# Optimization experiments

Measured on AMD Instinct MI355X. Metric: run time of the kernel, lower is better.

Reference implementation:

```python
import jax, jax.numpy as jnp
import numpy as np
from jax import lax

# ---- Haar (db1) wavelet filters, matching create_wavelet_filter ----
_S2 = float(1.0 / np.sqrt(2.0))
_dec_lo = np.array([_S2, _S2], np.float32)    # pywt dec_lo reversed (symmetric)
_dec_hi = np.array([_S2, -_S2], np.float32)   # pywt dec_hi [-s,s] reversed
_rec_lo = np.array([_S2, _S2], np.float32)    # pywt rec_lo flipped (symmetric)
_rec_hi = np.array([-_S2, _S2], np.float32)   # pywt rec_hi [s,-s] flipped

def _outer(a, b):  # torch: a.unsqueeze(0) * b.unsqueeze(1) -> [i,j] = a[j]*b[i]
    return b[:, None] * a[None, :]

DEC = jnp.asarray(np.stack([_outer(_dec_lo, _dec_lo), _outer(_dec_lo, _dec_hi),
                            _outer(_dec_hi, _dec_lo), _outer(_dec_hi, _dec_hi)]))  # [4,2,2]
REC = jnp.asarray(np.stack([_outer(_rec_lo, _rec_lo), _outer(_rec_lo, _rec_hi),
                            _outer(_rec_hi, _rec_lo), _outer(_rec_hi, _rec_hi)]))  # [4,2,2]

BN_EPS = 1e-5

def mish(x):
    return x * jnp.tanh(jax.nn.softplus(x))

def silu(x):
    return x * jax.nn.sigmoid(x)

def bn(x, g, b):  # eval-mode BatchNorm2d with running_mean=0, running_var=1
    return x * (g / jnp.sqrt(1.0 + BN_EPS))[None, :, None, None] + b[None, :, None, None]

def dwconv(x, w, pad):  # depthwise conv, w: [C,1,k,k]
    return lax.conv_general_dilated(x, w, (1, 1), [(pad, pad), (pad, pad)],
                                    feature_group_count=x.shape[1],
                                    dimension_numbers=('NCHW', 'OIHW', 'NCHW'))

def dyn_dwconv(x, ew, gw):
    # DynamicConv2d (depthwise experts). ew: [E,C,1,k,k], gw: [E,C]
    gates = jax.nn.softmax(x.mean((2, 3)) @ gw.T, axis=-1)  # [B,E]
    k = ew.shape[-1]
    outs = jnp.stack([dwconv(x, ew[e], k // 2) for e in range(ew.shape[0])], 1)  # [B,E,C,H,W]
    return jnp.einsum('be,bechw->bchw', gates, outs)

def local_branch(x, ew, gw, bn1g, bn1b, pw, bn2g, bn2b):
    # DWConv2d_BN_ReLU: dynamic dwconv -> BN -> Mish -> depthwise 1x1 (per-channel scale) -> BN
    y = mish(bn(dyn_dwconv(x, ew, gw), bn1g, bn1b))
    y = y * pw[None, :, None, None]
    return bn(y, bn2g, bn2b)

def sel_scan(u, xw, dtw, dtb, Alog, Dp):
    # u: [B,L,D]; xw: [R+2N,D]; dtw: [D,R]; dtb: [D]; Alog: [D,N]; Dp: [D]
    R = dtw.shape[1]
    N = Alog.shape[1]
    xdbl = jnp.einsum('bld,ed->ble', u, xw)
    dt, Bm, Cm = xdbl[..., :R], xdbl[..., R:R + N], xdbl[..., R + N:]
    delta = jax.nn.softplus(jnp.einsum('blr,dr->bld', dt, dtw) + dtb)  # [B,L,D]
    A = -jnp.exp(Alog)                                                  # [D,N]
    a = jnp.exp(delta[..., None] * A)                                   # [B,L,D,N]
    b = delta[..., None] * Bm[:, :, None, :] * u[..., None]             # [B,L,D,N]
    def comb(c1, c2):
        a1, b1 = c1
        a2, b2 = c2
        return a1 * a2, a2 * b1 + b2
    _, h = lax.associative_scan(comb, (a, b), axis=1)                    # h_t = a_t h_{t-1} + b_t
    return jnp.einsum('bldn,bln->bld', h, Cm) + Dp * u

def ss2d(x, in_w, cw, cb, xpw, dtw, dtb, Alog, Dp, ow):
    # SS2D (d_state=1, k_group=2, channel_first): in_proj -> dwconv+silu -> 2-direction
    # selective scan -> gate with silu(z) -> out_proj.
    B, C, H, W = x.shape
    xz = jnp.einsum('oc,bchw->bohw', in_w, x)
    d = in_w.shape[0] // 2
    xi, z = xz[:, :d], xz[:, d:]
    xc = silu(dwconv(xi, cw, 1) + cb[None, :, None, None])
    u0 = xc.reshape(B, d, H * W).transpose(0, 2, 1)                       # row-major scan
    u1 = xc.transpose(0, 1, 3, 2).reshape(B, d, H * W).transpose(0, 2, 1)  # col-major scan
    y0 = sel_scan(u0, xpw[0], dtw[0], dtb[0], Alog[0], Dp[0])
    y1 = sel_scan(u1, xpw[1], dtw[1], dtb[1], Alog[1], Dp[1])
    y0 = y0.transpose(0, 2, 1).reshape(B, d, H, W)
    y1 = y1.transpose(0, 2, 1).reshape(B, d, W, H).transpose(0, 1, 3, 2)
    y = (y0 + y1) * silu(z)
    return jnp.einsum('oc,bchw->bohw', ow, y)

def mbwt(x, wav_w, wav_b, wav_scale, base_scale,
         ss_in_w, ss_conv_w, ss_conv_b, ss_xproj_w, ss_dt_w, ss_dt_b, ss_A_log, ss_D, ss_out_w):
    # MBWTConv2d, wt_levels=1, H/W even. Haar WT (2x2 stride 2) == block reshape + einsum.
    B, C, H, W = x.shape
    xr = x.reshape(B, C, H // 2, 2, W // 2, 2)
    wt = jnp.einsum('bchpwq,kpq->bckhw', xr, DEC)                  # [B,C,4,h,w]
    tag = wt.reshape(B, 4 * C, H // 2, W // 2)
    tag = dwconv(tag, wav_w, wav_w.shape[-1] // 2) + wav_b[None, :, None, None]
    tag = (tag * wav_scale).reshape(B, C, 4, H // 2, W // 2)
    # inverse Haar WT (conv_transpose 2x2 stride 2, groups=C)
    up = jnp.einsum('bckhw,kpq->bchpwq', tag, REC).reshape(B, C, H, W)
    g = ss2d(x, ss_in_w, ss_conv_w, ss_conv_b, ss_xproj_w, ss_dt_w, ss_dt_b, ss_A_log, ss_D, ss_out_w)
    return base_scale * g + up


def setup_inputs() -> dict:
    key = jax.random.key(0)
    ks = iter(jax.random.split(key, 64))
    B, DIM, H, W = 16, 256, 64, 64
    Cg = Cl = 64
    d = {'x': jax.random.normal(next(ks), (B, DIM, H, W), jnp.float32)}
    for j, k in enumerate((3, 5, 7)):
        p = f'l{j}_'
        d[p + 'ew'] = jax.random.normal(next(ks), (4, Cl, 1, k, k), jnp.float32) * 0.1
        d[p + 'gw'] = jax.random.normal(next(ks), (4, Cl), jnp.float32) * 0.1
        d[p + 'bn1g'] = jnp.ones((Cl,), jnp.float32)
        d[p + 'bn1b'] = jnp.zeros((Cl,), jnp.float32)
        d[p + 'pw'] = jax.random.normal(next(ks), (Cl,), jnp.float32) * 0.2
        d[p + 'bn2g'] = jnp.ones((Cl,), jnp.float32)
        d[p + 'bn2b'] = jnp.zeros((Cl,), jnp.float32)
    d['wav_w'] = jax.random.normal(next(ks), (4 * Cg, 1, 3, 3), jnp.float32) * 0.1
    d['wav_b'] = jnp.zeros((4 * Cg,), jnp.float32)
    d['wav_scale'] = jnp.full((1, 4 * Cg, 1, 1), 0.1, jnp.float32)
    d['base_scale'] = jnp.ones((1, Cg, 1, 1), jnp.float32)
    dm, R, N, K = Cg, 4, 1, 2  # d_inner, dt_rank, d_state, k_group
    d['ss_in_w'] = jax.random.normal(next(ks), (2 * dm, Cg), jnp.float32) * float(1 / np.sqrt(Cg))
    d['ss_conv_w'] = jax.random.normal(next(ks), (dm, 1, 3, 3), jnp.float32) * 0.1
    d['ss_conv_b'] = jnp.zeros((dm,), jnp.float32)
    d['ss_xproj_w'] = jax.random.normal(next(ks), (K, R + 2 * N, dm), jnp.float32) * float(1 / np.sqrt(dm))
    d['ss_dt_w'] = jax.random.normal(next(ks), (K, dm, R), jnp.float32) * float(1 / np.sqrt(R))
    d['ss_dt_b'] = jnp.full((K, dm), -2.0, jnp.float32)
    d['ss_A_log'] = jnp.zeros((K, dm, N), jnp.float32)
    d['ss_D'] = jnp.ones((K, dm), jnp.float32)
    d['ss_out_w'] = jax.random.normal(next(ks), (Cg, dm), jnp.float32) * float(1 / np.sqrt(dm))
    return d


def reference(x,
              l0_ew, l0_gw, l0_bn1g, l0_bn1b, l0_pw, l0_bn2g, l0_bn2b,
              l1_ew, l1_gw, l1_bn1g, l1_bn1b, l1_pw, l1_bn2g, l1_bn2b,
              l2_ew, l2_gw, l2_bn1g, l2_bn1b, l2_pw, l2_bn2g, l2_bn2b,
              wav_w, wav_b, wav_scale, base_scale,
              ss_in_w, ss_conv_w, ss_conv_b, ss_xproj_w, ss_dt_w, ss_dt_b, ss_A_log, ss_D, ss_out_w):
    Cg, Cl = 64, 64
    xg, xl, xi = x[:, :Cg], x[:, Cg:Cg + Cl], x[:, Cg + Cl:]
    yl = (local_branch(xl, l0_ew, l0_gw, l0_bn1g, l0_bn1b, l0_pw, l0_bn2g, l0_bn2b)
          + local_branch(xl, l1_ew, l1_gw, l1_bn1g, l1_bn1b, l1_pw, l1_bn2g, l1_bn2b)
          + local_branch(xl, l2_ew, l2_gw, l2_bn1g, l2_bn1b, l2_pw, l2_bn2g, l2_bn2b))
    yg = mbwt(xg, wav_w, wav_b, wav_scale, base_scale,
              ss_in_w, ss_conv_w, ss_conv_b, ss_xproj_w, ss_dt_w, ss_dt_b, ss_A_log, ss_D, ss_out_w)
    return jnp.concatenate([yg, yl, xi], axis=1)
```

## Files before the change

kernel.cpp:

```cpp
#include <hip/hip_runtime.h>
#include <math.h>

static constexpr int NB   = 16;
static constexpr int DIM  = 256;
static constexpr int CG   = 64;
static constexpr int HH   = 64;
static constexpr int WW   = 64;
static constexpr int HW   = HH * WW;

__device__ __forceinline__ float mish_fast(float x) {
    float t = __expf(fminf(x, 20.f));
    float p = __builtin_fmaf(t, t, t + t);
    return x * p * __builtin_amdgcn_rcpf(p + 2.f);
}
__device__ __forceinline__ float silu_f(float x) {
    return x * __builtin_amdgcn_rcpf(1.f + __expf(-x));
}
__device__ __forceinline__ float softplus_fast(float x) {
    return fmaxf(x, 0.f) + __logf(1.f + __expf(-fabsf(x)));
}

__global__ __launch_bounds__(256) void k_stage1(
    const float* __restrict__ x,
    const float* __restrict__ wav_w, const float* __restrict__ wav_b,
    const float* __restrict__ wav_scale,
    float* __restrict__ up, float* __restrict__ mean,
    const float* __restrict__ in_w,
    float* __restrict__ xi, float* __restrict__ z) {
    __shared__ float smem[8192];
    int bid = blockIdx.x;
    int tid = threadIdx.x;

    if (bid % 3 != 2) {
        int aid = (bid / 3) * 2 + (bid % 3);
        int c = aid & 63, b = aid >> 6;
        float* wtb = smem;
        float* red = smem + 4352;
        const float* xp = x + ((size_t)b * DIM + c) * HW;

        {
            const float4* lp4 = (const float4*)(x + ((size_t)b * DIM + 64 + c) * HW);
            float s = 0.f;
            for (int i = tid; i < 1024; i += 256) {
                float4 v = lp4[i];
                s += (v.x + v.y) + (v.z + v.w);
            }
#pragma unroll
            for (int off = 32; off > 0; off >>= 1) s += __shfl_xor(s, off, 64);
            if ((tid & 63) == 0) red[tid >> 6] = s;
            __syncthreads();
            if (tid == 0)
                mean[b * 64 + c] = ((red[0] + red[1]) + (red[2] + red[3])) * (1.f / HW);
        }

#pragma unroll
        for (int it = 0; it < 2; ++it) {
            int p = tid + it * 256;
            int h = p >> 4, w2 = p & 15;
            float4 top = *(const float4*)(xp + (2 * h) * 64 + 4 * w2);
            float4 bot = *(const float4*)(xp + (2 * h + 1) * 64 + 4 * w2);
            float a0 = top.x, b0 = top.y, c0q = bot.x, d0 = bot.y;
            float a1 = top.z, b1 = top.w, c1q = bot.z, d1 = bot.w;
            int base0 = h * 34 + 2 * w2;
            *(float2*)(wtb + 0 * 1088 + base0) =
                make_float2(0.5f * (a0 + b0 + c0q + d0), 0.5f * (a1 + b1 + c1q + d1));
            *(float2*)(wtb + 1 * 1088 + base0) =
                make_float2(0.5f * (a0 + b0 - c0q - d0), 0.5f * (a1 + b1 - c1q - d1));
            *(float2*)(wtb + 2 * 1088 + base0) =
                make_float2(0.5f * (a0 - b0 + c0q - d0), 0.5f * (a1 - b1 + c1q - d1));
            *(float2*)(wtb + 3 * 1088 + base0) =
                make_float2(0.5f * (a0 - b0 - c0q + d0), 0.5f * (a1 - b1 - c1q + d1));
        }
        __syncthreads();

        float wk[4][9], tb[4];
#pragma unroll
        for (int k = 0; k < 4; ++k) {
            int ch = c * 4 + k;
            float sc = wav_scale[ch];
#pragma unroll
            for (int j = 0; j < 9; ++j) wk[k][j] = wav_w[ch * 9 + j] * sc;
            tb[k] = wav_b[ch] * sc;
        }
        float* upp = up + ((size_t)b * CG + c) * HW;
        for (int i = tid; i < 1024; i += 256) {
            int h = i >> 5, w = i & 31;
            float tg[4];
#pragma unroll
            for (int k = 0; k < 4; ++k) {
                float s = tb[k];
#pragma unroll
                for (int dy = -1; dy <= 1; ++dy) {
                    int hh = h + dy;
                    if (hh < 0 || hh >= 32) continue;
#pragma unroll
                    for (int dx = -1; dx <= 1; ++dx) {
                        int wx = w + dx;
                        if (wx < 0 || wx >= 32) continue;
                        s = fmaf(wtb[k * 1088 + hh * 34 + wx], wk[k][(dy + 1) * 3 + (dx + 1)], s);
                    }
                }
                tg[k] = s;
            }
            float u00 = 0.5f * (tg[0] - tg[1] - tg[2] + tg[3]);
            float u01 = 0.5f * (tg[0] - tg[1] + tg[2] - tg[3]);
            float u10 = 0.5f * (tg[0] + tg[1] - tg[2] - tg[3]);
            float u11 = 0.5f * (tg[0] + tg[1] + tg[2] + tg[3]);
            *(float2*)(upp + (2 * h) * 64 + 2 * w)     = make_float2(u00, u01);
            *(float2*)(upp + (2 * h + 1) * 64 + 2 * w) = make_float2(u10, u11);
        }
    } else {
        int id2 = bid / 3;
        int h0 = (id2 & 31) * 2;
        int b  = id2 >> 5;
        float* xs = smem;
        float* wt = smem + 4096;

        float acc[8][8];
#pragma unroll
        for (int i = 0; i < 8; ++i)
#pragma unroll
            for (int j = 0; j < 8; ++j) acc[i][j] = 0.f;

        int o0 = (tid >> 4) * 8;
        int p0 = (tid & 15) * 8;

        for (int ko = 0; ko < 64; ko += 32) {
            if (ko) __syncthreads();
            {
                int s = tid;
#pragma unroll
                for (int it = 0; it < 4; ++it, s += 256) {
                    int c = s >> 5, p4 = (s & 31) * 4;
                    float4 v = *(const float4*)(x + ((size_t)b * DIM + ko + c) * HW + h0 * 64 + p4);
                    *(float4*)(xs + c * 128 + p4) = v;
                }
            }
            {
                int s = tid;
#pragma unroll
                for (int it = 0; it < 4; ++it, s += 256) {
                    int o = s >> 3, c0 = (s & 7) * 4;
#pragma unroll
                    for (int i = 0; i < 4; ++i) {
                        int cc = c0 + i;
                        int osw = o ^ (((cc >> 2) & 3) << 3);
                        wt[cc * 128 + osw] = ((const float*)(in_w + o * 64 + ko + c0))[i];
                    }
                }
            }
            __syncthreads();
#pragma unroll 4
            for (int c = 0; c < 32; ++c) {
                int osw = o0 ^ (((c >> 2) & 3) << 3);
                float xv[8], wv[8];
                *(float4*)(xv)     = *(const float4*)(xs + c * 128 + p0);
                *(float4*)(xv + 4) = *(const float4*)(xs + c * 128 + p0 + 4);
                *(float4*)(wv)     = *(const float4*)(wt + c * 128 + osw);
                *(float4*)(wv + 4) = *(const float4*)(wt + c * 128 + osw + 4);
#pragma unroll
                for (int i = 0; i < 8; ++i)
#pragma unroll
                    for (int j = 0; j < 8; ++j)
                        acc[i][j] = fmaf(wv[i], xv[j], acc[i][j]);
            }
        }

#pragma unroll
        for (int i = 0; i < 8; ++i) {
            int o = o0 + i;
            float* dst = (o < 64) ? (xi + ((size_t)b * 64 + o) * HW + h0 * 64)
                                  : (z + ((size_t)b * 64 + (o - 64)) * HW + h0 * 64);
            *(float4*)(dst + p0)     = make_float4(acc[i][0], acc[i][1], acc[i][2], acc[i][3]);
            *(float4*)(dst + p0 + 4) = make_float4(acc[i][4], acc[i][5], acc[i][6], acc[i][7]);
        }
    }
}

__global__ __launch_bounds__(256) void k_stage2(
    const float* __restrict__ xi,
    const float* __restrict__ cw, const float* __restrict__ cb,
    const float* __restrict__ xpw,
    float* __restrict__ xc, float4* __restrict__ proj4, float2* __restrict__ projBC,
    const float* __restrict__ mean,
    const float* __restrict__ ew3, const float* __restrict__ gw3, const float* __restrict__ g13,
    const float* __restrict__ ew5, const float* __restrict__ gw5, const float* __restrict__ g15,
    const float* __restrict__ ew7, const float* __restrict__ gw7, const float* __restrict__ g17,
    float* __restrict__ w3o, float* __restrict__ w5o, float* __restrict__ w7o) {
    __shared__ float smem[12608];
    int bid = blockIdx.x;
    int tid = threadIdx.x;

    if (bid < 512) {
        int h0 = (bid & 31) * 2;
        int b  = bid >> 5;
        float* xs  = smem;
        float* xcs = smem + 8448;

        int dir = tid >> 7;
        int px  = tid & 127;
        float acc0 = 0.f, acc1 = 0.f, acc2 = 0.f, acc3 = 0.f, acc4 = 0.f, acc5 = 0.f;

        int cl_c = tid >> 3;
        int p0_c = (tid & 7) * 16;
        int row_c = p0_c >> 6;
        int wb_c  = p0_c & 63;

        for (int ch0 = 0; ch0 < 64; ch0 += 32) {
            if (ch0) __syncthreads();
            {
                int s = tid;
#pragma unroll
                for (int it = 0; it < 8; ++it, s += 256) {
                    int c = s >> 6;
                    int rem = s & 63;
                    int r = rem >> 4, w4 = (rem & 15) * 4;
                    int gh = h0 - 1 + r;
                    float4 v = make_float4(0.f, 0.f, 0.f, 0.f);
                    if (gh >= 0 && gh < 64)
                        v = *(const float4*)(xi + ((size_t)b * 64 + ch0 + c) * HW + gh * 64 + w4);
                    float* dp = xs + c * 264 + r * 66 + 1 + w4;
                    dp[0] = v.x; dp[1] = v.y; dp[2] = v.z; dp[3] = v.w;
                }
                if (tid < 128) {
                    int cl = tid >> 2, r = tid & 3;
                    xs[cl * 264 + r * 66 + 0]  = 0.f;
                    xs[cl * 264 + r * 66 + 65] = 0.f;
                }
            }
            __syncthreads();

            {
                float wk[9];
#pragma unroll
                for (int j = 0; j < 9; ++j) wk[j] = cw[(ch0 + cl_c) * 9 + j];
                float bias = cb[ch0 + cl_c];
                float accr[16];
#pragma unroll
                for (int k = 0; k < 16; ++k) accr[k] = bias;
#pragma unroll
                for (int dy = 0; dy < 3; ++dy) {
                    const float* rp = xs + cl_c * 264 + (row_c + dy) * 66 + wb_c;
                    float r[18];
#pragma unroll
                    for (int q = 0; q < 18; ++q) r[q] = rp[q];
#pragma unroll
                    for (int k = 0; k < 16; ++k)
#pragma unroll
                        for (int dx = 0; dx < 3; ++dx)
                            accr[k] = fmaf(r[k + dx], wk[dy * 3 + dx], accr[k]);
                }
#pragma unroll
                for (int k = 0; k < 16; ++k)
                    xcs[cl_c * 130 + p0_c + k] = silu_f(accr[k]);
            }
            __syncthreads();

            {
                int s = tid;
#pragma unroll
                for (int it = 0; it < 4; ++it, s += 256) {
                    int c = s >> 5, pq = (s & 31) * 4;
                    const float* sp = xcs + c * 130 + pq;
                    *(float4*)(xc + ((size_t)b * 64 + ch0 + c) * HW + h0 * 64 + pq) =
                        make_float4(sp[0], sp[1], sp[2], sp[3]);
                }
            }
            {
                const float* wp = xpw + dir * 6 * 64 + ch0;
#pragma unroll 8
                for (int c = 0; c < 32; ++c) {
                    float xv = xcs[c * 130 + px];
                    acc0 = fmaf(xv, wp[0 * 64 + c], acc0);
                    acc1 = fmaf(xv, wp[1 * 64 + c], acc1);
                    acc2 = fmaf(xv, wp[2 * 64 + c], acc2);
                    acc3 = fmaf(xv, wp[3 * 64 + c], acc3);
                    acc4 = fmaf(xv, wp[4 * 64 + c], acc4);
                    acc5 = fmaf(xv, wp[5 * 64 + c], acc5);
                }
            }
        }

        int h = h0 + (px >> 6), w = px & 63;
        int l = (dir == 0) ? (h * 64 + w) : (w * 64 + h);
        size_t base = ((size_t)dir * NB + b) * HW + l;
        proj4[base]  = make_float4(acc0, acc1, acc2, acc3);
        projBC[base] = make_float2(acc4, acc5);
    } else {
        int b = bid - 512;
        int c = tid;
        float* m = smem;
        float* g = smem + 64;
        if (c < 64) m[c] = mean[b * 64 + c];
        __syncthreads();
        const float rs = rsqrtf(1.f + 1e-5f);

#define WEFF_SECT(GW, EW, G1, OUT, K2)                                        \
        {                                                                     \
            if (c < 4) {                                                      \
                float l = 0.f;                                                \
                for (int cc = 0; cc < 64; ++cc) l += m[cc] * GW[c * 64 + cc]; \
                g[c] = l;                                                     \
            }                                                                 \
            __syncthreads();                                                  \
            if (c == 0) {                                                     \
                float mx = fmaxf(fmaxf(g[0], g[1]), fmaxf(g[2], g[3]));       \
                float e0 = expf(g[0] - mx), e1 = expf(g[1] - mx);             \
                float e2 = expf(g[2] - mx), e3 = expf(g[3] - mx);             \
                float inv = 1.f / (e0 + e1 + e2 + e3);                        \
                g[0] = e0 * inv; g[1] = e1 * inv; g[2] = e2 * inv; g[3] = e3 * inv; \
            }                                                                 \
            __syncthreads();                                                  \
            if (c < 64) {                                                     \
                float g1s = G1[c] * rs;                                       \
                for (int kk = 0; kk < K2; ++kk) {                             \
                    float w = 0.f;                                            \
                    for (int e = 0; e < 4; ++e) w += g[e] * EW[(e * 64 + c) * K2 + kk]; \
                    OUT[(b * 64 + c) * K2 + kk] = w * g1s;                    \
                }                                                             \
            }                                                                 \
            __syncthreads();                                                  \
        }

        WEFF_SECT(gw3, ew3, g13, w3o, 9)
        WEFF_SECT(gw5, ew5, g15, w5o, 25)
        WEFF_SECT(gw7, ew7, g17, w7o, 49)
#undef WEFF_SECT
    }
}

__global__ __launch_bounds__(256) void k_scan2(const float* __restrict__ xc,
                                               const float4* __restrict__ proj4,
                                               const float2* __restrict__ projBC,
                                               const float* __restrict__ dt_w,
                                               const float* __restrict__ dt_b,
                                               const float* __restrict__ A_log,
                                               const float* __restrict__ Dp,
                                               const float* __restrict__ z,
                                               float* __restrict__ yz) {
    int wave = threadIdx.x >> 6;
    int lane = threadIdx.x & 63;
    int wid = blockIdx.x;
    int b = wid >> 6;
    int d = wid & 63;

    __shared__ float ut[64 * 65];
    __shared__ float al[4][1088];
    __shared__ float bl[4][1088];
    __shared__ float aggA[4], aggB[4];

    const float* uplane = xc + ((size_t)b * 64 + d) * HW;
    const float4* up4 = (const float4*)uplane;
#pragma unroll
    for (int q = 0; q < 4; ++q) {
        int s = q * 256 + threadIdx.x;
        float4 v = up4[s];
        int r = s >> 4, c0 = (s & 15) * 4;
        float* p = ut + r * 65 + c0;
        p[0] = v.x; p[1] = v.y; p[2] = v.z; p[3] = v.w;
    }
    __syncthreads();

    int ch = wave;
    float* a_my = al[wave];
    float* b_my = bl[wave];
    float y0r[16];

    {
        float4 wv = *(const float4*)(dt_w + d * 4);
        float db = dt_b[d];
        float A = -__expf(A_log[d]);
        float Dv = Dp[d];
        const float4* p4 = proj4 + (size_t)b * HW;
        const float2* pBC = projBC + (size_t)b * HW;

        float uv[16], cm[16];
#pragma unroll
        for (int j = 0; j < 16; ++j) {
            int el = j * 64 + lane;
            int e  = ch * 1024 + el;
            float4 t4 = p4[e];
            float2 t2 = pBC[e];
            float u = ut[(ch * 16 + j) * 65 + lane];
            uv[j] = u; cm[j] = t2.y;
            float pre = fmaf(t4.x, wv.x, fmaf(t4.y, wv.y,
                        fmaf(t4.z, wv.z, fmaf(t4.w, wv.w, db))));
            float delta = softplus_fast(pre);
            float aj = __expf(delta * A);
            float bj = delta * t2.x * u;
            int idx = (el >> 4) * 17 + (el & 15);
            a_my[idx] = aj;
            b_my[idx] = bj;
        }
        __builtin_amdgcn_wave_barrier();

        float a[16], bb[16];
#pragma unroll
        for (int j = 0; j < 16; ++j) {
            a[j]  = a_my[lane * 17 + j];
            bb[j] = b_my[lane * 17 + j];
        }
        float As = 1.f, Bs = 0.f;
#pragma unroll
        for (int j = 0; j < 16; ++j) { Bs = fmaf(a[j], Bs, bb[j]); As *= a[j]; }
        float Ai = As, Bi = Bs;
#pragma unroll
        for (int off = 1; off < 64; off <<= 1) {
            float ap = __shfl_up(Ai, (unsigned)off, 64);
            float bp = __shfl_up(Bi, (unsigned)off, 64);
            if (lane >= off) { Bi = fmaf(Ai, bp, Bi); Ai *= ap; }
        }
        if (lane == 63) { aggA[wave] = Ai; aggB[wave] = Bi; }
        __syncthreads();
        float carry = 0.f;
        for (int k = 0; k < wave; ++k) carry = fmaf(aggA[k], carry, aggB[k]);
        float ap1 = __shfl_up(Ai, 1, 64);
        float bp1 = __shfl_up(Bi, 1, 64);
        float h = (lane == 0) ? carry : fmaf(ap1, carry, bp1);
#pragma unroll
        for (int j = 0; j < 16; ++j) {
            h = fmaf(a[j], h, bb[j]);
            a_my[lane * 17 + j] = h;
        }
        __builtin_amdgcn_wave_barrier();
#pragma unroll
        for (int j = 0; j < 16; ++j) {
            int el = j * 64 + lane;
            float hv = a_my[(el >> 4) * 17 + (el & 15)];
            y0r[j] = fmaf(hv, cm[j], Dv * uv[j]);
        }
    }
    __syncthreads();

    {
        int pd = 64 + d;
        float4 wv = *(const float4*)(dt_w + pd * 4);
        float db = dt_b[pd];
        float A = -__expf(A_log[pd]);
        float Dv = Dp[pd];
        const float4* p4 = proj4 + ((size_t)NB + b) * HW;
        const float2* pBC = projBC + ((size_t)NB + b) * HW;

        float uv[16], cm[16];
#pragma unroll
        for (int j = 0; j < 16; ++j) {
            int el = j * 64 + lane;
            int e  = ch * 1024 + el;
            float4 t4 = p4[e];
            float2 t2 = pBC[e];
            float u = ut[lane * 65 + (ch * 16 + j)];
            uv[j] = u; cm[j] = t2.y;
            float pre = fmaf(t4.x, wv.x, fmaf(t4.y, wv.y,
                        fmaf(t4.z, wv.z, fmaf(t4.w, wv.w, db))));
            float delta = softplus_fast(pre);
            float aj = __expf(delta * A);
            float bj = delta * t2.x * u;
            int idx = (el >> 4) * 17 + (el & 15);
            a_my[idx] = aj;
            b_my[idx] = bj;
        }
        __builtin_amdgcn_wave_barrier();

        float a[16], bb[16];
#pragma unroll
        for (int j = 0; j < 16; ++j) {
            a[j]  = a_my[lane * 17 + j];
            bb[j] = b_my[lane * 17 + j];
        }
        float As = 1.f, Bs = 0.f;
#pragma unroll
        for (int j = 0; j < 16; ++j) { Bs = fmaf(a[j], Bs, bb[j]); As *= a[j]; }
        float Ai = As, Bi = Bs;
#pragma unroll
        for (int off = 1; off < 64; off <<= 1) {
            float ap = __shfl_up(Ai, (unsigned)off, 64);
            float bp = __shfl_up(Bi, (unsigned)off, 64);
            if (lane >= off) { Bi = fmaf(Ai, bp, Bi); Ai *= ap; }
        }
        if (lane == 63) { aggA[wave] = Ai; aggB[wave] = Bi; }
        __syncthreads();
        float carry = 0.f;
        for (int k = 0; k < wave; ++k) carry = fmaf(aggA[k], carry, aggB[k]);
        float ap1 = __shfl_up(Ai, 1, 64);
        float bp1 = __shfl_up(Bi, 1, 64);
        float h = (lane == 0) ? carry : fmaf(ap1, carry, bp1);
#pragma unroll
        for (int j = 0; j < 16; ++j) {
            h = fmaf(a[j], h, bb[j]);
            a_my[lane * 17 + j] = h;
        }
        __builtin_amdgcn_wave_barrier();
#pragma unroll
        for (int j = 0; j < 16; ++j) {
            int el = j * 64 + lane;
            float hv = a_my[(el >> 4) * 17 + (el & 15)];
            ut[lane * 65 + (ch * 16 + j)] = fmaf(hv, cm[j], Dv * uv[j]);
        }
    }
    __syncthreads();

    const float* zp = z + ((size_t)b * 64 + d) * HW;
    float* yp = yz + ((size_t)b * 64 + d) * HW;
#pragma unroll
    for (int j = 0; j < 16; ++j) {
        int e = ch * 1024 + j * 64 + lane;
        float y1v = ut[(ch * 16 + j) * 65 + lane];
        float zz = zp[e];
        yp[e] = (y0r[j] + y1v) * silu_f(zz);
    }
}

__global__ __launch_bounds__(256) void k_stage4(
    const float* __restrict__ x,
    const float* __restrict__ w3, const float* __restrict__ w5, const float* __restrict__ w7,
    const float* __restrict__ b1_0, const float* __restrict__ pw0,
    const float* __restrict__ g2_0, const float* __restrict__ b2_0,
    const float* __restrict__ b1_1, const float* __restrict__ pw1,
    const float* __restrict__ g2_1, const float* __restrict__ b2_1,
    const float* __restrict__ b1_2, const float* __restrict__ pw2,
    const float* __restrict__ g2_2, const float* __restrict__ b2_2,
    const float* __restrict__ yz, const float* __restrict__ ow,
    const float* __restrict__ base_scale, const float* __restrict__ up,
    float* __restrict__ out) {
    __shared__ float smem[6144];
    int bid = blockIdx.x;
    int tid = threadIdx.x;

    if (bid % 5 != 4) {
        int cidx = (bid / 5) * 4 + (bid % 5);
        int half = cidx & 1;
        int c = (cidx >> 1) & 63;
        int b = cidx >> 7;
        int oy = half * 32;
        float* t = smem;
        const float* xp = x + ((size_t)b * DIM + 64 + c) * HW;

        {
            float4 z4 = make_float4(0.f, 0.f, 0.f, 0.f);
            for (int i = tid; i < 684; i += 256) ((float4*)t)[i] = z4;
        }
        {
            const float4* x4 = (const float4*)x;
            float4* o4 = (float4*)out;
            int base = cidx * 1024;
#pragma unroll
            for (int it = 0; it < 4; ++it) {
                int idx = base + it * 256 + tid;
                int bb = idx >> 17;
                int r  = idx & 131071;
                int gi = bb * 262144 + 131072 + r;
                o4[gi] = x4[gi];
            }
        }
        __syncthreads();
        {
            for (int i = tid; i < 608; i += 256) {
                int tr = i >> 4, q = (i & 15) * 4;
                int gy = oy + tr - 3;
                if (gy >= 0 && gy < 64)
                    *(float4*)(t + tr * 72 + 4 + q) = *(const float4*)(xp + gy * 64 + q);
            }
        }
        const float* w3p = w3 + (b * 64 + c) * 9;
        const float* w5p = w5 + (b * 64 + c) * 25;
        const float* w7p = w7 + (b * 64 + c) * 49;
        float W3r[9], W5r[25], W7r[49];
#pragma unroll
        for (int j = 0; j < 9; ++j)  W3r[j] = w3p[j];
#pragma unroll
        for (int j = 0; j < 25; ++j) W5r[j] = w5p[j];
#pragma unroll
        for (int j = 0; j < 49; ++j) W7r[j] = w7p[j];
        __syncthreads();

        const float rs = rsqrtf(1.f + 1e-5f);
        float bb1a = b1_0[c], bb1b = b1_1[c], bb1c = b1_2[c];
        float ssa = pw0[c] * g2_0[c] * rs, ssb = pw1[c] * g2_1[c] * rs, ssc = pw2[c] * g2_2[c] * rs;
        float bb2a = b2_0[c], bb2b = b2_1[c], bb2c = b2_2[c];

        int r  = tid >> 4;
        int x0 = (tid & 15) * 4;

        float a3[2][4] = {{0.f,0.f,0.f,0.f},{0.f,0.f,0.f,0.f}};
        float a5[2][4] = {{0.f,0.f,0.f,0.f},{0.f,0.f,0.f,0.f}};
        float a7[2][4] = {{0.f,0.f,0.f,0.f},{0.f,0.f,0.f,0.f}};

#pragma unroll
        for (int j = 0; j < 8; ++j) {
            const float4* rp = (const float4*)(t + (2 * r + j) * 72 + x0);
            float4 q0 = rp[0], q1 = rp[1], q2 = rp[2];
            float rr[12] = {q0.x, q0.y, q0.z, q0.w, q1.x, q1.y, q1.z, q1.w,
                            q2.x, q2.y, q2.z, q2.w};
            if (j <= 6) {
#pragma unroll
                for (int k = 0; k < 4; ++k)
#pragma unroll
                    for (int dx = 0; dx < 7; ++dx)
                        a7[0][k] = fmaf(rr[k + dx + 1], W7r[j * 7 + dx], a7[0][k]);
                if (j >= 1 && j <= 5) {
#pragma unroll
                    for (int k = 0; k < 4; ++k)
#pragma unroll
                        for (int dx = 0; dx < 5; ++dx)
                            a5[0][k] = fmaf(rr[k + dx + 2], W5r[(j - 1) * 5 + dx], a5[0][k]);
                }
                if (j >= 2 && j <= 4) {
#pragma unroll
                    for (int k = 0; k < 4; ++k)
#pragma unroll
                        for (int dx = 0; dx < 3; ++dx)
                            a3[0][k] = fmaf(rr[k + dx + 3], W3r[(j - 2) * 3 + dx], a3[0][k]);
                }
            }
            if (j >= 1) {
#pragma unroll
                for (int k = 0; k < 4; ++k)
#pragma unroll
                    for (int dx = 0; dx < 7; ++dx)
                        a7[1][k] = fmaf(rr[k + dx + 1], W7r[(j - 1) * 7 + dx], a7[1][k]);
                if (j >= 2 && j <= 6) {
#pragma unroll
                    for (int k = 0; k < 4; ++k)
#pragma unroll
                        for (int dx = 0; dx < 5; ++dx)
                            a5[1][k] = fmaf(rr[k + dx + 2], W5r[(j - 2) * 5 + dx], a5[1][k]);
                }
                if (j >= 3 && j <= 5) {
#pragma unroll
                    for (int k = 0; k < 4; ++k)
#pragma unroll
                        for (int dx = 0; dx < 3; ++dx)
                            a3[1][k] = fmaf(rr[k + dx + 3], W3r[(j - 3) * 3 + dx], a3[1][k]);
                }
            }
        }

        float* op = out + ((size_t)b * DIM + 64 + c) * HW;
#pragma unroll
        for (int rr2 = 0; rr2 < 2; ++rr2) {
            float4 res;
            float* rv = (float*)&res;
#pragma unroll
            for (int k = 0; k < 4; ++k) {
                rv[k] = mish_fast(a3[rr2][k] + bb1a) * ssa + bb2a
                      + mish_fast(a5[rr2][k] + bb1b) * ssb + bb2b
                      + mish_fast(a7[rr2][k] + bb1c) * ssc + bb2c;
            }
            *(float4*)(op + (oy + 2 * r + rr2) * 64 + x0) = res;
        }
    } else {
        int id2 = bid / 5;
        int h0 = (id2 & 31) * 2;
        int b  = id2 >> 5;
        float* yv = smem;
        float* wt = smem + 4096;

        float acc[8][4];
#pragma unroll
        for (int i = 0; i < 8; ++i)
#pragma unroll
            for (int j = 0; j < 4; ++j) acc[i][j] = 0.f;

        int o0 = (tid >> 5) * 8;
        int p0 = (tid & 31) * 4;

        for (int ko = 0; ko < 64; ko += 32) {
            if (ko) __syncthreads();
            {
                int s = tid;
#pragma unroll
                for (int it = 0; it < 4; ++it, s += 256) {
                    int c = s >> 5, p4 = (s & 31) * 4;
                    size_t idx = ((size_t)b * 64 + ko + c) * HW + h0 * 64 + p4;
                    *(float4*)(yv + c * 128 + p4) = *(const float4*)(yz + idx);
                }
            }
            {
                int s = tid;
#pragma unroll
                for (int it = 0; it < 2; ++it, s += 256) {
                    int o = s >> 3, c0 = (s & 7) * 4;
#pragma unroll
                    for (int i = 0; i < 4; ++i) {
                        int cc = c0 + i;
                        int osw = o ^ (((cc >> 2) & 3) << 3);
                        wt[cc * 64 + osw] = ((const float*)(ow + o * 64 + ko + c0))[i];
                    }
                }
            }
            __syncthreads();
#pragma unroll 4
            for (int c = 0; c < 32; ++c) {
                int osw = o0 ^ (((c >> 2) & 3) << 3);
                float wv[8], xv[4];
                *(float4*)(wv)     = *(const float4*)(wt + c * 64 + osw);
                *(float4*)(wv + 4) = *(const float4*)(wt + c * 64 + osw + 4);
                *(float4*)(xv)     = *(const float4*)(yv + c * 128 + p0);
#pragma unroll
                for (int i = 0; i < 8; ++i)
#pragma unroll
                    for (int j = 0; j < 4; ++j)
                        acc[i][j] = fmaf(wv[i], xv[j], acc[i][j]);
            }
        }

#pragma unroll
        for (int i = 0; i < 8; ++i) {
            int o = o0 + i;
            float bs = base_scale[o];
            float4 u = *(const float4*)(up + ((size_t)b * 64 + o) * HW + h0 * 64 + p0);
            float4 r = make_float4(fmaf(bs, acc[i][0], u.x),
                                   fmaf(bs, acc[i][1], u.y),
                                   fmaf(bs, acc[i][2], u.z),
                                   fmaf(bs, acc[i][3], u.w));
            *(float4*)(out + ((size_t)b * DIM + o) * HW + h0 * 64 + p0) = r;
        }
    }
}

extern "C" void kernel_launch(void* const* d_in, const int* in_sizes, int n_in,
                              void* d_out, int out_size, void* d_ws, size_t ws_size,
                              hipStream_t stream) {
    (void)in_sizes; (void)n_in; (void)out_size; (void)ws_size;
    const float* x = (const float*)d_in[0];
    float* out = (float*)d_out;
    float* ws = (float*)d_ws;

    const size_t IMG = (size_t)NB * 64 * HW;
    float* buf_xi   = ws;
    float* buf_z    = ws + IMG;
    float* buf_xc   = ws + 2 * IMG;
    float* buf_up   = ws + 3 * IMG;
    float* buf_p4   = ws + 4 * IMG;
    float* buf_pBC  = buf_p4 + (size_t)4 * 2 * NB * HW;
    float* buf_mean = buf_pBC + (size_t)2 * 2 * NB * HW;
    float* buf_w3   = buf_mean + 1024;
    float* buf_w5   = buf_w3 + 16 * 64 * 9;
    float* buf_w7   = buf_w5 + 16 * 64 * 25;

    k_stage1<<<1536, 256, 0, stream>>>(x,
        (const float*)d_in[22], (const float*)d_in[23], (const float*)d_in[24],
        buf_up, buf_mean,
        (const float*)d_in[26], buf_xi, buf_z);

    k_stage2<<<528, 256, 0, stream>>>(buf_xi,
        (const float*)d_in[27], (const float*)d_in[28], (const float*)d_in[29],
        buf_xc, (float4*)buf_p4, (float2*)buf_pBC,
        buf_mean,
        (const float*)d_in[1],  (const float*)d_in[2],  (const float*)d_in[3],
        (const float*)d_in[8],  (const float*)d_in[9],  (const float*)d_in[10],
        (const float*)d_in[15], (const float*)d_in[16], (const float*)d_in[17],
        buf_w3, buf_w5, buf_w7);

    k_scan2<<<1024, 256, 0, stream>>>(buf_xc, (const float4*)buf_p4, (const float2*)buf_pBC,
        (const float*)d_in[30], (const float*)d_in[31],
        (const float*)d_in[32], (const float*)d_in[33],
        buf_z, buf_xi);

    k_stage4<<<2560, 256, 0, stream>>>(x, buf_w3, buf_w5, buf_w7,
        (const float*)d_in[4],  (const float*)d_in[5],  (const float*)d_in[6],  (const float*)d_in[7],
        (const float*)d_in[11], (const float*)d_in[12], (const float*)d_in[13], (const float*)d_in[14],
        (const float*)d_in[18], (const float*)d_in[19], (const float*)d_in[20], (const float*)d_in[21],
        buf_xi, (const float*)d_in[34], (const float*)d_in[25], buf_up, out);
}
```

Measured before the change: 114.3 us.

## Split stage1 wavelet blocks by row half and shrink GEMM K-tile

The wavelet/mean part of stage1 now splits each channel's work into two row halves, with a one-row halo in the LDS tile. Each half writes its own partial mean, and stage2 sums the two. The in_w GEMM path drops its K-chunk from 32 to 16 and vectorises the weight load, which halves LDS use to 16KB. The block count grows from 1536 to 2560 for more parallelism and occupancy, at the cost of redundant halo loads and extra syncs.

```diff
diff --git a/kernel.cpp b/kernel.cpp
--- a/kernel.cpp
+++ b/kernel.cpp
@@ -24,25 +24,30 @@
     const float* __restrict__ x,
     const float* __restrict__ wav_w, const float* __restrict__ wav_b,
     const float* __restrict__ wav_scale,
-    float* __restrict__ up, float* __restrict__ mean,
+    float* __restrict__ up, float* __restrict__ meanp,
     const float* __restrict__ in_w,
     float* __restrict__ xi, float* __restrict__ z) {
-    __shared__ float smem[8192];
+    __shared__ float smem[4096];
     int bid = blockIdx.x;
     int tid = threadIdx.x;
 
-    if (bid % 3 != 2) {
-        int aid = (bid / 3) * 2 + (bid % 3);
-        int c = aid & 63, b = aid >> 6;
+    if (bid % 5 != 4) {
+        int aid = (bid / 5) * 4 + (bid % 5);
+        int half = aid & 1;
+        int c = (aid >> 1) & 63;
+        int b = aid >> 7;
+        int hs = half * 16;
         float* wtb = smem;
-        float* red = smem + 4352;
+        float* red = smem + 2448;
         const float* xp = x + ((size_t)b * DIM + c) * HW;
 
         {
-            const float4* lp4 = (const float4*)(x + ((size_t)b * DIM + 64 + c) * HW);
+            const float4* lp4 = (const float4*)(x + ((size_t)b * DIM + 64 + c) * HW
+                                                + half * 32 * 64);
             float s = 0.f;
-            for (int i = tid; i < 1024; i += 256) {
-                float4 v = lp4[i];
+#pragma unroll
+            for (int it = 0; it < 2; ++it) {
+                float4 v = lp4[tid + it * 256];
                 s += (v.x + v.y) + (v.z + v.w);
             }
 #pragma unroll
@@ -50,26 +55,32 @@
             if ((tid & 63) == 0) red[tid >> 6] = s;
             __syncthreads();
             if (tid == 0)
-                mean[b * 64 + c] = ((red[0] + red[1]) + (red[2] + red[3])) * (1.f / HW);
+                meanp[half * 1024 + b * 64 + c] =
+                    ((red[0] + red[1]) + (red[2] + red[3])) * (1.f / HW);
         }
 
 #pragma unroll
         for (int it = 0; it < 2; ++it) {
             int p = tid + it * 256;
-            int h = p >> 4, w2 = p & 15;
-            float4 top = *(const float4*)(xp + (2 * h) * 64 + 4 * w2);
-            float4 bot = *(const float4*)(xp + (2 * h + 1) * 64 + 4 * w2);
-            float a0 = top.x, b0 = top.y, c0q = bot.x, d0 = bot.y;
-            float a1 = top.z, b1 = top.w, c1q = bot.z, d1 = bot.w;
-            int base0 = h * 34 + 2 * w2;
-            *(float2*)(wtb + 0 * 1088 + base0) =
-                make_float2(0.5f * (a0 + b0 + c0q + d0), 0.5f * (a1 + b1 + c1q + d1));
-            *(float2*)(wtb + 1 * 1088 + base0) =
-                make_float2(0.5f * (a0 + b0 - c0q - d0), 0.5f * (a1 + b1 - c1q - d1));
-            *(float2*)(wtb + 2 * 1088 + base0) =
-                make_float2(0.5f * (a0 - b0 + c0q - d0), 0.5f * (a1 - b1 + c1q - d1));
-            *(float2*)(wtb + 3 * 1088 + base0) =
-                make_float2(0.5f * (a0 - b0 - c0q + d0), 0.5f * (a1 - b1 - c1q + d1));
+            if (p < 288) {
+                int tr = p >> 4, w2 = p & 15;
+                int hr = hs - 1 + tr;
+                if (hr >= 0 && hr < 32) {
+                    float4 top = *(const float4*)(xp + (2 * hr) * 64 + 4 * w2);
+                    float4 bot = *(const float4*)(xp + (2 * hr + 1) * 64 + 4 * w2);
+                    float a0 = top.x, b0 = top.y, c0q = bot.x, d0 = bot.y;
+                    float a1 = top.z, b1 = top.w, c1q = bot.z, d1 = bot.w;
+                    int base0 = tr * 34 + 2 * w2;
+                    *(float2*)(wtb + 0 * 612 + base0) =
+                        make_float2(0.5f * (a0 + b0 + c0q + d0), 0.5f * (a1 + b1 + c1q + d1));
+                    *(float2*)(wtb + 1 * 612 + base0) =
+                        make_float2(0.5f * (a0 + b0 - c0q - d0), 0.5f * (a1 + b1 - c1q - d1));
+                    *(float2*)(wtb + 2 * 612 + base0) =
+                        make_float2(0.5f * (a0 - b0 + c0q - d0), 0.5f * (a1 - b1 + c1q - d1));
+                    *(float2*)(wtb + 3 * 612 + base0) =
+                        make_float2(0.5f * (a0 - b0 - c0q + d0), 0.5f * (a1 - b1 - c1q + d1));
+                }
+            }
         }
         __syncthreads();
 
@@ -83,8 +94,11 @@
             tb[k] = wav_b[ch] * sc;
         }
         float* upp = up + ((size_t)b * CG + c) * HW;
-        for (int i = tid; i < 1024; i += 256) {
-            int h = i >> 5, w = i & 31;
+#pragma unroll
+        for (int it = 0; it < 2; ++it) {
+            int i = tid + it * 256;
+            int hl = i >> 5, w = i & 31;
+            int h = hs + hl;
             float tg[4];
 #pragma unroll
             for (int k = 0; k < 4; ++k) {
@@ -93,11 +107,12 @@
                 for (int dy = -1; dy <= 1; ++dy) {
                     int hh = h + dy;
                     if (hh < 0 || hh >= 32) continue;
+                    int trr = hh - (hs - 1);
 #pragma unroll
                     for (int dx = -1; dx <= 1; ++dx) {
                         int wx = w + dx;
                         if (wx < 0 || wx >= 32) continue;
-                        s = fmaf(wtb[k * 1088 + hh * 34 + wx], wk[k][(dy + 1) * 3 + (dx + 1)], s);
+                        s = fmaf(wtb[k * 612 + trr * 34 + wx], wk[k][(dy + 1) * 3 + (dx + 1)], s);
                     }
                 }
                 tg[k] = s;
@@ -110,11 +125,11 @@
             *(float2*)(upp + (2 * h + 1) * 64 + 2 * w) = make_float2(u10, u11);
         }
     } else {
-        int id2 = bid / 3;
-        int h0 = (id2 & 31) * 2;
-        int b  = id2 >> 5;
+        int did = bid / 5;
+        int h0 = (did & 31) * 2;
+        int b  = did >> 5;
         float* xs = smem;
-        float* wt = smem + 4096;
+        float* wt = smem + 2048;
 
         float acc[8][8];
 #pragma unroll
@@ -125,12 +140,12 @@
         int o0 = (tid >> 4) * 8;
         int p0 = (tid & 15) * 8;
 
-        for (int ko = 0; ko < 64; ko += 32) {
+        for (int ko = 0; ko < 64; ko += 16) {
             if (ko) __syncthreads();
             {
                 int s = tid;
 #pragma unroll
-                for (int it = 0; it < 4; ++it, s += 256) {
+                for (int it = 0; it < 2; ++it, s += 256) {
                     int c = s >> 5, p4 = (s & 31) * 4;
                     float4 v = *(const float4*)(x + ((size_t)b * DIM + ko + c) * HW + h0 * 64 + p4);
                     *(float4*)(xs + c * 128 + p4) = v;
@@ -139,19 +154,20 @@
             {
                 int s = tid;
 #pragma unroll
-                for (int it = 0; it < 4; ++it, s += 256) {
-                    int o = s >> 3, c0 = (s & 7) * 4;
+                for (int it = 0; it < 2; ++it, s += 256) {
+                    int o = s >> 2, c0 = (s & 3) * 4;
+                    float4 v = *(const float4*)(in_w + o * 64 + ko + c0);
 #pragma unroll
                     for (int i = 0; i < 4; ++i) {
                         int cc = c0 + i;
                         int osw = o ^ (((cc >> 2) & 3) << 3);
-                        wt[cc * 128 + osw] = ((const float*)(in_w + o * 64 + ko + c0))[i];
+                        wt[cc * 128 + osw] = ((const float*)&v)[i];
                     }
                 }
             }
             __syncthreads();
 #pragma unroll 4
-            for (int c = 0; c < 32; ++c) {
+            for (int c = 0; c < 16; ++c) {
                 int osw = o0 ^ (((c >> 2) & 3) << 3);
                 float xv[8], wv[8];
                 *(float4*)(xv)     = *(const float4*)(xs + c * 128 + p0);
@@ -182,7 +198,7 @@
     const float* __restrict__ cw, const float* __restrict__ cb,
     const float* __restrict__ xpw,
     float* __restrict__ xc, float4* __restrict__ proj4, float2* __restrict__ projBC,
-    const float* __restrict__ mean,
+    const float* __restrict__ meanp,
     const float* __restrict__ ew3, const float* __restrict__ gw3, const float* __restrict__ g13,
     const float* __restrict__ ew5, const float* __restrict__ gw5, const float* __restrict__ g15,
     const float* __restrict__ ew7, const float* __restrict__ gw7, const float* __restrict__ g17,
@@ -291,7 +307,7 @@
         int c = tid;
         float* m = smem;
         float* g = smem + 64;
-        if (c < 64) m[c] = mean[b * 64 + c];
+        if (c < 64) m[c] = meanp[b * 64 + c] + meanp[1024 + b * 64 + c];
         __syncthreads();
         const float rs = rsqrtf(1.f + 1e-5f);
 
@@ -734,11 +750,11 @@
     float* buf_p4   = ws + 4 * IMG;
     float* buf_pBC  = buf_p4 + (size_t)4 * 2 * NB * HW;
     float* buf_mean = buf_pBC + (size_t)2 * 2 * NB * HW;
-    float* buf_w3   = buf_mean + 1024;
+    float* buf_w3   = buf_mean + 2048;
     float* buf_w5   = buf_w3 + 16 * 64 * 9;
     float* buf_w7   = buf_w5 + 16 * 64 * 25;
 
-    k_stage1<<<1536, 256, 0, stream>>>(x,
+    k_stage1<<<2560, 256, 0, stream>>>(x,
         (const float*)d_in[22], (const float*)d_in[23], (const float*)d_in[24],
         buf_up, buf_mean,
         (const float*)d_in[26], buf_xi, buf_z);
```

Result: no change. 114.1 us, median of 2 (-0.2%).
